# Optimization experiments

Hardware: AMD Instinct MI355X
Metric: run time of the kernel (lower is better)

## Reference

```python
import jax, jax.numpy as jnp
import numpy as np
import math

B, S, D, H, DFF, NB = 16, 512, 512, 8, 2048, 2
DK = D // H
L = 3 * NB  # NB blocks_1 layers + 2*NB blocks_2 layers
NEG = -1e32
LN_EPS = 1e-5


def _layernorm(x, g, b):
    mu = jnp.mean(x, -1, keepdims=True)
    var = jnp.mean((x - mu) ** 2, -1, keepdims=True)
    return (x - mu) * jax.lax.rsqrt(var + LN_EPS) * g + b


def _attention(q, k, v, mask, gamma, zero_pad):
    # q,k,v: [B,H,S,DK]; mask: [S,S] bool; gamma: [H]
    scores = jnp.einsum('bhid,bhjd->bhij', q, k) / math.sqrt(DK)
    maskf = mask.astype(scores.dtype)
    # no-grad distance-decay block (torch.no_grad + .detach())
    p = jax.nn.softmax(jnp.where(mask, scores, NEG), axis=-1) * maskf
    distcum = jnp.cumsum(p, axis=-1)
    disttot = jnp.sum(p, axis=-1, keepdims=True)
    idx = jnp.arange(S, dtype=scores.dtype)
    pos = jnp.abs(idx[None, :] - idx[:, None])  # |i-j|, [S,S]
    dist = jnp.sqrt(jnp.clip((disttot - distcum) * pos, 0.0, None))
    dist = jax.lax.stop_gradient(dist)
    g = -jax.nn.softplus(gamma)[None, :, None, None]  # [1,H,1,1]
    total_effect = jnp.clip(jnp.exp(dist * g), 1e-5, 1e5)
    scores = jnp.where(mask, scores * total_effect, NEG)
    attn = jax.nn.softmax(scores, axis=-1)
    if zero_pad:
        attn = attn.at[:, :, 0, :].set(0.0)
    return jnp.einsum('bhij,bhjd->bhid', attn, v)


def _mha(q, k, v, mask, zero_pad, Wk, bk, Wv, bv, Wo, bo, gam):
    # kq_same=True: queries also use the k projection
    def proj(x, W, b):
        return (x @ W + b).reshape(B, S, H, DK).transpose(0, 2, 1, 3)
    qh = proj(q, Wk, bk)
    kh = proj(k, Wk, bk)
    vh = proj(v, Wv, bv)
    out = _attention(qh, kh, vh, mask, gam, zero_pad)
    out = out.transpose(0, 2, 1, 3).reshape(B, S, D)
    return out @ Wo + bo


def _layer(mask_flag, query, key_, values, apply_pos, p):
    (Wk, bk, Wv, bv, Wo, bo, gam, g1, bn1, W1, bf1, W2, bf2, g2, bn2) = p
    idx = jnp.arange(S)
    if mask_flag == 1:
        mask = idx[None, :] <= idx[:, None]  # peek current + past
    else:
        mask = idx[None, :] < idx[:, None]   # strictly past
    zero_pad = (mask_flag == 0)
    q2 = _mha(query, key_, values, mask, zero_pad, Wk, bk, Wv, bv, Wo, bo, gam)
    query = _layernorm(query + q2, g1, bn1)
    if apply_pos:
        q2 = jax.nn.relu(query @ W1 + bf1) @ W2 + bf2
        query = _layernorm(query + q2, g2, bn2)
    return query


def _forward(q_embed_data, qa_embed_data, pid_embed_data, params):
    # emb_type='qid' (no 'pdiff') -> pid_embed_data unused inside attention
    def pslice(l):
        return tuple(a[l] for a in params)
    y = qa_embed_data
    x = q_embed_data
    for l in range(NB):  # blocks_1: self-attn on y, mask=1
        y = _layer(1, y, y, y, True, pslice(l))
    for i in range(NB):  # blocks_2: alternating (mask=1, no FFN) / (mask=0, values=y)
        x = _layer(1, x, x, x, False, pslice(NB + 2 * i))
        x = _layer(0, x, x, y, True, pslice(NB + 2 * i + 1))
    return x, y


def setup_inputs() -> dict:
    key = jax.random.key(0)
    ks = jax.random.split(key, 10)
    sD = 1.0 / math.sqrt(D)
    sF = 1.0 / math.sqrt(DFF)
    f32 = jnp.float32
    return {
        'q_embed_data': jax.random.normal(ks[0], (B, S, D), f32),
        'qa_embed_data': jax.random.normal(ks[1], (B, S, D), f32),
        'pid_embed_data': jax.random.normal(ks[2], (B, S, D), f32),
        'Wk': jax.random.normal(ks[3], (L, D, D), f32) * sD,
        'bk': jnp.zeros((L, D), f32),
        'Wv': jax.random.normal(ks[4], (L, D, D), f32) * sD,
        'bv': jnp.zeros((L, D), f32),
        'Wo': jax.random.normal(ks[5], (L, D, D), f32) * sD,
        'bo': jnp.zeros((L, D), f32),
        'gammas': jax.random.normal(ks[6], (L, H), f32) * 0.5,
        'ln1_g': jnp.ones((L, D), f32),
        'ln1_b': jnp.zeros((L, D), f32),
        'W1': jax.random.normal(ks[7], (L, D, DFF), f32) * sD,
        'b1': jnp.zeros((L, DFF), f32),
        'W2': jax.random.normal(ks[8], (L, DFF, D), f32) * sF,
        'b2': jnp.zeros((L, D), f32),
        'ln2_g': jnp.ones((L, D), f32),
        'ln2_b': jnp.zeros((L, D), f32),
    }


def reference(q_embed_data, qa_embed_data, pid_embed_data, Wk, bk, Wv, bv, Wo, bo,
              gammas, ln1_g, ln1_b, W1, b1, W2, b2, ln2_g, ln2_b):
    params = (Wk, bk, Wv, bv, Wo, bo, gammas, ln1_g, ln1_b, W1, b1, W2, b2, ln2_g, ln2_b)
    x, y = _forward(q_embed_data, qa_embed_data, pid_embed_data, params)
    return (x, y)
```

## Files before the change

### kernel.cpp

```cpp
#include <hip/hip_runtime.h>
#include <hip/hip_bf16.h>

#define Bsz  16
#define Sl   512
#define Dm   512
#define Hn   8
#define DKh  64
#define DFFn 2048
#define MROWS (Bsz * Sl)
#define NEGV (-1e32f)

typedef _Float16 f16;
typedef f16 f16x8 __attribute__((ext_vector_type(8)));
typedef f16 f16x4 __attribute__((ext_vector_type(4)));
typedef float f32x4 __attribute__((ext_vector_type(4)));

#define GLDS16(g, l) __builtin_amdgcn_global_load_lds( \
    (const __attribute__((address_space(1))) void*)(g), \
    (__attribute__((address_space(3))) void*)(l), 16, 0, 0)

__global__ void k_copy2(const float* __restrict__ in, float* __restrict__ out,
                        f16* __restrict__ outh, int n) {
    int i = blockIdx.x * 256 + threadIdx.x;
    if (i < n) { float v = in[i]; out[i] = v; outh[i] = (f16)v; }
}

__global__ void k_bcat(const float* __restrict__ bk, const float* __restrict__ bv,
                       float* __restrict__ bkv) {
    int i = blockIdx.x * 256 + threadIdx.x;
    int z = i >> 10, c = i & 1023;
    bkv[i] = (c < 512) ? bk[z * 512 + c] : bv[z * 512 + c - 512];
}

__global__ __launch_bounds__(256) void k_wconv(const float* __restrict__ src,
        f16* __restrict__ dst, int K, int N, int lmap, size_t zstride)
{
    __shared__ float T[32][36];
    int z = blockIdx.z;
    int ls = lmap ? (z < 2 ? z : 2 * z - 1) : z;
    const float* S = src + (size_t)ls * K * N;
    f16* Dt = dst + (size_t)z * zstride;
    int n0 = blockIdx.x * 32, k0 = blockIdx.y * 32;
    int t = threadIdx.x;
    int r = t >> 3, c = (t & 7) * 4;
    float4 v = *(const float4*)(S + (size_t)(k0 + r) * N + n0 + c);
    T[r][c] = v.x; T[r][c + 1] = v.y; T[r][c + 2] = v.z; T[r][c + 3] = v.w;
    __syncthreads();
    int n = t >> 3, kq = (t & 7) * 4;
    f16x4 o = { (f16)T[kq][n], (f16)T[kq + 1][n], (f16)T[kq + 2][n], (f16)T[kq + 3][n] };
    *(f16x4*)(Dt + (size_t)(n0 + n) * K + k0 + kq) = o;
}

template <int RELU, int OUT16, int VTOUT, int BK64>
__global__ __launch_bounds__(256) void k_gemm(
    const f16* __restrict__ A, const f16* __restrict__ Bt,
    const float* __restrict__ bias, float* __restrict__ C, f16* __restrict__ Ch,
    int M, int N, int K)
{
    constexpr int HL = BK64 ? 2 : 1;
    constexpr int BUF = HL * 4096;
    __shared__ f16 As[2 * BUF];
    __shared__ f16 Bs[2 * BUF];
    int tid = threadIdx.x;
    int w = tid >> 6, lane = tid & 63;
    int ln = lane & 15, rg = lane >> 4;
    int wr = w >> 1, wc = w & 1;
    int m0 = blockIdx.y * 128, n0 = blockIdx.x * 128;

    int s0 = tid, s1 = 256 + tid;
    int r0s = s0 >> 2, c0s = ((s0 & 3) ^ ((s0 >> 3) & 3));
    int r1s = s1 >> 2, c1s = ((s1 & 3) ^ ((s1 >> 3) & 3));

    const f16* a0 = A + (size_t)(m0 + r0s) * K + c0s * 8;
    const f16* a1 = A + (size_t)(m0 + r1s) * K + c1s * 8;
    const f16* b0 = Bt + (size_t)(n0 + r0s) * K + c0s * 8;
    const f16* b1 = Bt + (size_t)(n0 + r1s) * K + c1s * 8;

    int cc8 = (rg ^ ((ln >> 1) & 3)) * 8;

    f32x4 acc[4][4] = {};

    int nk = K >> (BK64 ? 6 : 5);

    auto STAGE = [&](int nb, int kt) {
        f16* lA = As + nb * BUF + w * 512;
        f16* lB = Bs + nb * BUF + w * 512;
        GLDS16(a0 + kt, lA);
        GLDS16(a1 + kt, lA + 2048);
        GLDS16(b0 + kt, lB);
        GLDS16(b1 + kt, lB + 2048);
        if (BK64) {
            GLDS16(a0 + kt + 32, lA + 4096);
            GLDS16(a1 + kt + 32, lA + 4096 + 2048);
            GLDS16(b0 + kt + 32, lB + 4096);
            GLDS16(b1 + kt + 32, lB + 4096 + 2048);
        }
    };

    STAGE(0, 0);
    __syncthreads();

    int cur = 0;
    for (int t = 0; t < nk; ++t) {
        if (t + 1 < nk) STAGE(cur ^ 1, (t + 1) << (BK64 ? 6 : 5));

#pragma unroll
        for (int hh = 0; hh < HL; ++hh) {
            const f16* Ab = As + cur * BUF + hh * 4096;
            const f16* Bb = Bs + cur * BUF + hh * 4096;
            f16x8 af[4], bf[4];
#pragma unroll
            for (int i = 0; i < 4; ++i) {
                int m = wr * 64 + i * 16 + ln;
                af[i] = *(const f16x8*)(Ab + m * 32 + cc8);
                int nn = wc * 64 + i * 16 + ln;
                bf[i] = *(const f16x8*)(Bb + nn * 32 + cc8);
            }
#pragma unroll
            for (int i = 0; i < 4; ++i)
#pragma unroll
                for (int j = 0; j < 4; ++j)
                    acc[i][j] = __builtin_amdgcn_mfma_f32_16x16x32_f16(af[i], bf[j], acc[i][j], 0, 0, 0);
        }

        __syncthreads();
        cur ^= 1;
    }

#pragma unroll
    for (int j = 0; j < 4; ++j) {
        int col = n0 + wc * 64 + j * 16 + ln;
        float bj = bias[col];
#pragma unroll
        for (int i = 0; i < 4; ++i) {
            int rb = m0 + wr * 64 + i * 16 + rg * 4;
            if (VTOUT == 1) {
                int bq = rb >> 9, s = rb & 511;
                int hh = col >> 6, dk = col & 63;
                f16x4 o;
#pragma unroll
                for (int r = 0; r < 4; ++r) o[r] = (f16)(acc[i][j][r] + bj);
                *(f16x4*)(Ch + (((size_t)(bq * 8 + hh) * 64 + dk) << 9) + s) = o;
            } else if (VTOUT == 2) {
                if (n0 < 512) {
#pragma unroll
                    for (int r = 0; r < 4; ++r)
                        Ch[(size_t)(rb + r) * 512 + col] = (f16)(acc[i][j][r] + bj);
                } else {
                    f16* Cv = (f16*)C;
                    int colv = col - 512;
                    int bq = rb >> 9, s = rb & 511;
                    int hh = colv >> 6, dk = colv & 63;
                    f16x4 o;
#pragma unroll
                    for (int r = 0; r < 4; ++r) o[r] = (f16)(acc[i][j][r] + bj);
                    *(f16x4*)(Cv + (((size_t)(bq * 8 + hh) * 64 + dk) << 9) + s) = o;
                }
            } else {
#pragma unroll
                for (int r = 0; r < 4; ++r) {
                    float v = acc[i][j][r] + bj;
                    if (RELU) v = fmaxf(v, 0.f);
                    if (OUT16) Ch[(size_t)(rb + r) * N + col] = (f16)v;
                    else       C [(size_t)(rb + r) * N + col] = v;
                }
            }
        }
    }
}

template <int JTC>
__device__ __forceinline__ void attn_body(
    float (*Sc)[516], f16* Ph, const f16* Qbase, const f16* vbase, f16* ob,
    f16x8 aq0, f16x8 aq1, float g,
    int w, int lane, int ln, int rg, int i0, int maskflag)
{
#pragma unroll
    for (int ui = 0; ui < JTC; ++ui) {
        int u = w + ui * 4;
        const f16* kb = Qbase + (size_t)(u * 16 + ln) * Dm + rg * 8;
        f16x8 b0 = *(const f16x8*)(kb);
        f16x8 b1 = *(const f16x8*)(kb + 32);
        f32x4 c = {};
        c = __builtin_amdgcn_mfma_f32_16x16x32_f16(aq0, b0, c, 0, 0, 0);
        c = __builtin_amdgcn_mfma_f32_16x16x32_f16(aq1, b1, c, 0, 0, 0);
#pragma unroll
        for (int r = 0; r < 4; ++r)
            Sc[rg * 4 + r][u * 16 + ln] = c[r];
    }
    __syncthreads();

    int jbase = lane * JTC;
    int im = i0 + w * 4;

    float run[4];
#pragma unroll
    for (int q = 0; q < 4; ++q) {
        int jmax = maskflag ? (im + q) : (im + q - 1);
        float acc = 0.f;
#pragma unroll
        for (int k = 0; k < JTC; ++k) {
            int j = jbase + k;
            float s = (j <= jmax) ? Sc[w * 4 + q][j] * 0.125f : NEGV;
            acc += __expf(s);
        }
        run[q] = acc;
    }
    float sl[4] = { run[0], run[1], run[2], run[3] };
#pragma unroll
    for (int off = 1; off < 64; off <<= 1) {
        float n0 = __shfl_up(sl[0], off);
        float n1 = __shfl_up(sl[1], off);
        float n2 = __shfl_up(sl[2], off);
        float n3 = __shfl_up(sl[3], off);
        if (lane >= off) { sl[0] += n0; sl[1] += n1; sl[2] += n2; sl[3] += n3; }
    }

    float pe2s[4][JTC];
    float Z2[4];
#pragma unroll
    for (int q = 0; q < 4; ++q) {
        float excl = sl[q] - run[q];
        float Z = __shfl(sl[q], 63);
        float inv = 1.f / Z;
        int i = im + q;
        int jmax = maskflag ? i : (i - 1);
        float csum = 0.f, z2 = 0.f;
#pragma unroll
        for (int k = 0; k < JTC; ++k) {
            int j = jbase + k;
            float s = (j <= jmax) ? Sc[w * 4 + q][j] * 0.125f : NEGV;
            float pe = __expf(s);
            csum += pe;
            float rem = (Z - excl - csum) * inv;
            float pos = fabsf((float)(i - j));
            float dd = fmaxf(rem * pos, 0.f);
            float te = __expf(sqrtf(dd) * g);
            te = fminf(fmaxf(te, 1e-5f), 1e5f);
            float sc = (j <= jmax) ? s * te : NEGV;
            float pe2 = __expf(sc);
            pe2s[q][k] = pe2;
            z2 += pe2;
        }
        Z2[q] = z2;
    }
#pragma unroll
    for (int off = 32; off >= 1; off >>= 1) {
        Z2[0] += __shfl_xor(Z2[0], off);
        Z2[1] += __shfl_xor(Z2[1], off);
        Z2[2] += __shfl_xor(Z2[2], off);
        Z2[3] += __shfl_xor(Z2[3], off);
    }
    __syncthreads();

#pragma unroll
    for (int q = 0; q < 4; ++q) {
        int r = w * 4 + q;
        float inv2 = 1.f / Z2[q];
        int zp = (maskflag == 0) && (im + q == 0);
        if constexpr (JTC == 8) {
            int slot = (lane & ~7) | ((lane & 7) ^ (r & 7));
            f16x8 o8;
#pragma unroll
            for (int k = 0; k < 8; ++k)
                o8[k] = (f16)(zp ? 0.f : pe2s[q][k] * inv2);
            *(f16x8*)(Ph + r * 512 + slot * 8) = o8;
        } else if constexpr (JTC == 4) {
            int cj = lane >> 1;
            int slot = (cj & ~7) | ((cj & 7) ^ (r & 7));
            f16x4 o4;
#pragma unroll
            for (int k = 0; k < 4; ++k)
                o4[k] = (f16)(zp ? 0.f : pe2s[q][k] * inv2);
            *(f16x4*)(Ph + r * 512 + slot * 8 + (lane & 1) * 4) = o4;
        } else {
#pragma unroll
            for (int k = 0; k < JTC; ++k) {
                int j = jbase + k;
                int cj = j >> 3;
                int slot = (cj & ~7) | ((cj & 7) ^ (r & 7));
                Ph[r * 512 + slot * 8 + (j & 7)] =
                    (f16)(zp ? 0.f : pe2s[q][k] * inv2);
            }
        }
    }
    __syncthreads();

    f32x4 oa0 = {}, oa1 = {};
#pragma unroll
    for (int f = 0; f < 2 * JTC; ++f) {
        f16x8 bv = *(const f16x8*)(vbase + (f >> 1) * 64 + (f & 1) * 32);
        int c = (f >> 1) * 8 + (f & 1) * 4 + rg;
        int slot = (c & ~7) | ((c & 7) ^ (ln & 7));
        f16x8 ap = *(const f16x8*)(Ph + ln * 512 + slot * 8);
        if (f & 1) oa1 = __builtin_amdgcn_mfma_f32_16x16x32_f16(ap, bv, oa1, 0, 0, 0);
        else       oa0 = __builtin_amdgcn_mfma_f32_16x16x32_f16(ap, bv, oa0, 0, 0, 0);
    }
    f32x4 oa = oa0 + oa1;
#pragma unroll
    for (int r = 0; r < 4; ++r)
        ob[(size_t)r * Dm] = (f16)oa[r];
}

__global__ __launch_bounds__(256, 4) void k_attn(
    const f16* __restrict__ Qh, const f16* __restrict__ VT,
    f16* __restrict__ O, const float* __restrict__ gam, int maskflag)
{
    __shared__ float Sc[16][516];
    f16* Ph = (f16*)Sc;

    int tid = threadIdx.x;
    int w = tid >> 6, lane = tid & 63;
    int ln = lane & 15, rg = lane >> 4;

    int bid = blockIdx.x;
    int lbid = (bid & 7) * 512 + (bid >> 3);
    int tile = 31 - (lbid & 31);
    int bh = lbid >> 5;
    int b = bh >> 3, h = bh & 7;
    int i0 = tile * 16;
    int jtc = (tile >> 2) + 1;

    const f16* Qbase = Qh + ((size_t)b * Sl) * Dm + h * DKh;
    const f16* vbase = VT + ((size_t)bh * 64 + w * 16 + ln) * 512 + rg * 8;
    f16* ob = O + ((size_t)b * Sl + i0 + rg * 4) * Dm + h * DKh + w * 16 + ln;

    float gm = gam[h];
    float g = -((gm > 20.f) ? gm : log1pf(__expf(gm)));

    f16x8 aq0 = *(const f16x8*)(Qbase + (size_t)(i0 + ln) * Dm + rg * 8);
    f16x8 aq1 = *(const f16x8*)(Qbase + (size_t)(i0 + ln) * Dm + 32 + rg * 8);

    switch (jtc) {
    case 1: attn_body<1>(Sc, Ph, Qbase, vbase, ob, aq0, aq1, g, w, lane, ln, rg, i0, maskflag); break;
    case 2: attn_body<2>(Sc, Ph, Qbase, vbase, ob, aq0, aq1, g, w, lane, ln, rg, i0, maskflag); break;
    case 3: attn_body<3>(Sc, Ph, Qbase, vbase, ob, aq0, aq1, g, w, lane, ln, rg, i0, maskflag); break;
    case 4: attn_body<4>(Sc, Ph, Qbase, vbase, ob, aq0, aq1, g, w, lane, ln, rg, i0, maskflag); break;
    case 5: attn_body<5>(Sc, Ph, Qbase, vbase, ob, aq0, aq1, g, w, lane, ln, rg, i0, maskflag); break;
    case 6: attn_body<6>(Sc, Ph, Qbase, vbase, ob, aq0, aq1, g, w, lane, ln, rg, i0, maskflag); break;
    case 7: attn_body<7>(Sc, Ph, Qbase, vbase, ob, aq0, aq1, g, w, lane, ln, rg, i0, maskflag); break;
    default: attn_body<8>(Sc, Ph, Qbase, vbase, ob, aq0, aq1, g, w, lane, ln, rg, i0, maskflag); break;
    }
}

__global__ __launch_bounds__(256) void k_ln(
    const float* __restrict__ Xn, const float* __restrict__ Rr,
    const float* __restrict__ gw, const float* __restrict__ bw,
    float* __restrict__ Out, f16* __restrict__ Outh)
{
    int tid = threadIdx.x;
    int w = tid >> 6, lane = tid & 63;
    int row = blockIdx.x * 4 + w;
    const float* xr = Xn + (size_t)row * Dm;
    const float* rr = Rr + (size_t)row * Dm;
    int c0 = lane * 4, c1 = 256 + lane * 4;
    float4 va = *(const float4*)(xr + c0);
    float4 vb = *(const float4*)(xr + c1);
    float4 ra = *(const float4*)(rr + c0);
    float4 rb = *(const float4*)(rr + c1);
    va.x += ra.x; va.y += ra.y; va.z += ra.z; va.w += ra.w;
    vb.x += rb.x; vb.y += rb.y; vb.z += rb.z; vb.w += rb.w;
    float sum = va.x + va.y + va.z + va.w + vb.x + vb.y + vb.z + vb.w;
#pragma unroll
    for (int off = 32; off >= 1; off >>= 1) sum += __shfl_xor(sum, off);
    float mu = sum * (1.f / 512.f);
    float var = 0.f;
    {
        float d;
        d = va.x - mu; var += d * d;  d = va.y - mu; var += d * d;
        d = va.z - mu; var += d * d;  d = va.w - mu; var += d * d;
        d = vb.x - mu; var += d * d;  d = vb.y - mu; var += d * d;
        d = vb.z - mu; var += d * d;  d = vb.w - mu; var += d * d;
    }
#pragma unroll
    for (int off = 32; off >= 1; off >>= 1) var += __shfl_xor(var, off);
    float rs = rsqrtf(var * (1.f / 512.f) + 1e-5f);
    float4 ga = *(const float4*)(gw + c0);
    float4 gb = *(const float4*)(gw + c1);
    float4 ba = *(const float4*)(bw + c0);
    float4 bb = *(const float4*)(bw + c1);
    float4 oa, ob;
    oa.x = (va.x - mu) * rs * ga.x + ba.x;  oa.y = (va.y - mu) * rs * ga.y + ba.y;
    oa.z = (va.z - mu) * rs * ga.z + ba.z;  oa.w = (va.w - mu) * rs * ga.w + ba.w;
    ob.x = (vb.x - mu) * rs * gb.x + bb.x;  ob.y = (vb.y - mu) * rs * gb.y + bb.y;
    ob.z = (vb.z - mu) * rs * gb.z + bb.z;  ob.w = (vb.w - mu) * rs * gb.w + bb.w;
    float* orow = Out + (size_t)row * Dm;
    f16* ohrow = Outh + (size_t)row * Dm;
    *(float4*)(orow + c0) = oa;
    *(float4*)(orow + c1) = ob;
    f16x4 ha = { (f16)oa.x, (f16)oa.y, (f16)oa.z, (f16)oa.w };
    f16x4 hb = { (f16)ob.x, (f16)ob.y, (f16)ob.z, (f16)ob.w };
    *(f16x4*)(ohrow + c0) = ha;
    *(f16x4*)(ohrow + c1) = hb;
}

extern "C" void kernel_launch(void* const* d_in, const int* in_sizes, int n_in,
                              void* d_out, int out_size, void* d_ws, size_t ws_size,
                              hipStream_t stream)
{
    const float* q_emb  = (const float*)d_in[0];
    const float* qa_emb = (const float*)d_in[1];
    const float* Wk  = (const float*)d_in[3];
    const float* bk  = (const float*)d_in[4];
    const float* Wv  = (const float*)d_in[5];
    const float* bv  = (const float*)d_in[6];
    const float* Wo  = (const float*)d_in[7];
    const float* bo  = (const float*)d_in[8];
    const float* gam = (const float*)d_in[9];
    const float* l1g = (const float*)d_in[10];
    const float* l1b = (const float*)d_in[11];
    const float* W1  = (const float*)d_in[12];
    const float* b1  = (const float*)d_in[13];
    const float* W2  = (const float*)d_in[14];
    const float* b2  = (const float*)d_in[15];
    const float* l2g = (const float*)d_in[16];
    const float* l2b = (const float*)d_in[17];
    float* outp = (float*)d_out;

    const size_t NE  = (size_t)MROWS * Dm;
    const size_t WDD = (size_t)Dm * Dm;
    const size_t WDF = (size_t)Dm * DFFn;
    const size_t WKV = 2 * WDD;

    float* xbuf = (float*)d_ws;
    float* ybuf = xbuf + NE;
    float* t2   = ybuf + NE;
    f16* xh  = (f16*)(t2 + NE);
    f16* yh  = xh + NE;
    f16* R   = yh + NE;
    f16* qh  = R;
    f16* vt  = R + 2 * NE;
    f16* t1h = R + 3 * NE;
    f16* fbh = R;
    f16* wkvh = R + 4 * NE;
    f16* woh = wkvh + 6 * WKV;
    f16* w1h = woh + 6 * WDD;
    f16* w2h = w1h + 4 * WDF;
    float* bkv = (float*)(w2h + 4 * WDF);

    k_wconv<<<dim3(Dm / 32, Dm / 32, 6), 256, 0, stream>>>(Wk, wkvh, Dm, Dm, 0, WKV);
    k_wconv<<<dim3(Dm / 32, Dm / 32, 6), 256, 0, stream>>>(Wv, wkvh + WDD, Dm, Dm, 0, WKV);
    k_wconv<<<dim3(Dm / 32, Dm / 32, 6), 256, 0, stream>>>(Wo, woh, Dm, Dm, 0, WDD);
    k_wconv<<<dim3(DFFn / 32, Dm / 32, 4), 256, 0, stream>>>(W1, w1h, Dm, DFFn, 1, WDF);
    k_wconv<<<dim3(Dm / 32, DFFn / 32, 4), 256, 0, stream>>>(W2, w2h, DFFn, Dm, 1, WDF);
    k_bcat<<<24, 256, 0, stream>>>(bk, bv, bkv);

    const int n = (int)NE;
    k_copy2<<<n / 256, 256, 0, stream>>>(q_emb,  xbuf, xh, n);
    k_copy2<<<n / 256, 256, 0, stream>>>(qa_emb, ybuf, yh, n);

    auto gemm32 = [&](const f16* A, const f16* Bt, const float* bias, float* C,
                      int M, int N, int K) {
        k_gemm<0, 0, 0, 1><<<dim3(N / 128, M / 128), 256, 0, stream>>>(A, Bt, bias, C, nullptr, M, N, K);
    };

    auto layer = [&](int l, int maskflag, float* Xq, f16* Xqh, f16* Xvh,
                     bool apply_pos, float* finalOut) {
        if (Xqh == Xvh) {
            k_gemm<0, 1, 2, 1><<<dim3(1024 / 128, MROWS / 128), 256, 0, stream>>>(
                Xqh, wkvh + (size_t)l * WKV, bkv + l * 1024, (float*)vt, qh, MROWS, 1024, Dm);
        } else {
            k_gemm<0, 1, 0, 1><<<dim3(Dm / 128, MROWS / 128), 256, 0, stream>>>(
                Xqh, wkvh + (size_t)l * WKV, bk + l * Dm, nullptr, qh, MROWS, Dm, Dm);
            k_gemm<0, 1, 1, 1><<<dim3(Dm / 128, MROWS / 128), 256, 0, stream>>>(
                Xvh, wkvh + (size_t)l * WKV + WDD, bv + l * Dm, nullptr, vt, MROWS, Dm, Dm);
        }
        k_attn<<<Bsz * Hn * 32, 256, 0, stream>>>(qh, vt, t1h, gam + l * Hn, maskflag);
        gemm32(t1h, woh + (size_t)l * WDD, bo + l * Dm, t2, MROWS, Dm, Dm);
        if (apply_pos) {
            k_ln<<<MROWS / 4, 256, 0, stream>>>(t2, Xq, l1g + l * Dm, l1b + l * Dm, Xq, Xqh);
            int sl = (l < 2) ? l : ((l + 1) >> 1);
            k_gemm<1, 1, 0, 0><<<dim3(DFFn / 128, MROWS / 128), 256, 0, stream>>>(
                Xqh, w1h + (size_t)sl * WDF, b1 + l * DFFn, nullptr, fbh, MROWS, DFFn, Dm);
            k_gemm<0, 0, 0, 1><<<dim3(Dm / 128, MROWS / 128), 256, 0, stream>>>(
                fbh, w2h + (size_t)sl * WDF, b2 + l * Dm, t2, nullptr, MROWS, Dm, DFFn);
            k_ln<<<MROWS / 4, 256, 0, stream>>>(t2, Xq, l2g + l * Dm, l2b + l * Dm,
                                                finalOut ? finalOut : Xq, Xqh);
        } else {
            k_ln<<<MROWS / 4, 256, 0, stream>>>(t2, Xq, l1g + l * Dm, l1b + l * Dm,
                                                finalOut ? finalOut : Xq, Xqh);
        }
    };

    const size_t NEo = NE;
    layer(0, 1, ybuf, yh, yh, true, nullptr);
    layer(1, 1, ybuf, yh, yh, true, outp + NEo);
    layer(2, 1, xbuf, xh, xh, false, nullptr);
    layer(3, 0, xbuf, xh, yh, true, nullptr);
    layer(4, 1, xbuf, xh, xh, false, nullptr);
    layer(5, 0, xbuf, xh, yh, true, outp);
}
```

Before: 1.136 ms.

## Merge prep kernels, fuse split Q/V projection GEMMs, cache attention scores in registers

Eight setup launches (weight transpose/convert, bias concat, embedding copies) are merged into one flat-indexed prep kernel. For layers whose query and value inputs differ, the two separate projection GEMMs become one launch that picks its A matrix, weight and bias by block index. In attention, each lane's score row is read once from shared memory into registers with vector loads, and the masked exponentials are reused in the second pass instead of being reloaded and recomputed. This cuts launch overhead, shared-memory reads and repeated math, at the cost of more registers per thread in the attention kernel.

```diff
diff --git a/kernel.cpp b/kernel.cpp
--- a/kernel.cpp
+++ b/kernel.cpp
@@ -19,29 +19,21 @@
     (const __attribute__((address_space(1))) void*)(g), \
     (__attribute__((address_space(3))) void*)(l), 16, 0, 0)
 
-__global__ void k_copy2(const float* __restrict__ in, float* __restrict__ out,
-                        f16* __restrict__ outh, int n) {
-    int i = blockIdx.x * 256 + threadIdx.x;
-    if (i < n) { float v = in[i]; out[i] = v; outh[i] = (f16)v; }
-}
-
-__global__ void k_bcat(const float* __restrict__ bk, const float* __restrict__ bv,
-                       float* __restrict__ bkv) {
-    int i = blockIdx.x * 256 + threadIdx.x;
-    int z = i >> 10, c = i & 1023;
-    bkv[i] = (c < 512) ? bk[z * 512 + c] : bv[z * 512 + c - 512];
-}
-
-__global__ __launch_bounds__(256) void k_wconv(const float* __restrict__ src,
-        f16* __restrict__ dst, int K, int N, int lmap, size_t zstride)
-{
-    __shared__ float T[32][36];
-    int z = blockIdx.z;
+struct PrepArgs {
+    const float *Wk, *Wv, *Wo, *W1, *W2, *bk, *bv, *q_emb, *qa_emb;
+    f16 *wkvh, *woh, *w1h, *w2h;
+    float *bkv, *xbuf, *ybuf;
+    f16 *xh, *yh;
+};
+
+__device__ __forceinline__ void wconv_body(const float* src, f16* dst,
+        int K, int N, int lmap, size_t zstride, int z, int nx, int ny,
+        int t, float (*T)[36])
+{
     int ls = lmap ? (z < 2 ? z : 2 * z - 1) : z;
     const float* S = src + (size_t)ls * K * N;
     f16* Dt = dst + (size_t)z * zstride;
-    int n0 = blockIdx.x * 32, k0 = blockIdx.y * 32;
-    int t = threadIdx.x;
+    int n0 = nx * 32, k0 = ny * 32;
     int r = t >> 3, c = (t & 7) * 4;
     float4 v = *(const float4*)(S + (size_t)(k0 + r) * N + n0 + c);
     T[r][c] = v.x; T[r][c + 1] = v.y; T[r][c + 2] = v.z; T[r][c + 3] = v.w;
@@ -51,11 +43,53 @@
     *(f16x4*)(Dt + (size_t)(n0 + n) * K + k0 + kq) = o;
 }
 
+__global__ __launch_bounds__(256) void k_prep(PrepArgs a)
+{
+    __shared__ float T[32][36];
+    int id = blockIdx.x;
+    int t = threadIdx.x;
+    const size_t WDD = (size_t)Dm * Dm;
+    const size_t WDF = (size_t)Dm * DFFn;
+    const size_t WKV = 2 * WDD;
+
+    if (id < 4608) {
+        int which = id / 1536, rest = id % 1536;
+        int z = rest >> 8, r2 = rest & 255;
+        int nx = r2 & 15, ny = r2 >> 4;
+        if (which == 0)      wconv_body(a.Wk, a.wkvh,       Dm, Dm, 0, WKV, z, nx, ny, t, T);
+        else if (which == 1) wconv_body(a.Wv, a.wkvh + WDD, Dm, Dm, 0, WKV, z, nx, ny, t, T);
+        else                 wconv_body(a.Wo, a.woh,        Dm, Dm, 0, WDD, z, nx, ny, t, T);
+    } else if (id < 8704) {
+        int id2 = id - 4608;
+        int z = id2 >> 10, r2 = id2 & 1023;
+        int nx = r2 & 63, ny = r2 >> 6;
+        wconv_body(a.W1, a.w1h, Dm, DFFn, 1, WDF, z, nx, ny, t, T);
+    } else if (id < 12800) {
+        int id3 = id - 8704;
+        int z = id3 >> 10, r2 = id3 & 1023;
+        int nx = r2 & 15, ny = r2 >> 4;
+        wconv_body(a.W2, a.w2h, DFFn, Dm, 1, WDF, z, nx, ny, t, T);
+    } else if (id < 12824) {
+        int i = (id - 12800) * 256 + t;
+        int z = i >> 10, c = i & 1023;
+        a.bkv[i] = (c < 512) ? a.bk[z * 512 + c] : a.bv[z * 512 + c - 512];
+    } else if (id < 29208) {
+        int i = (id - 12824) * 256 + t;
+        float v = a.q_emb[i];
+        a.xbuf[i] = v; a.xh[i] = (f16)v;
+    } else {
+        int i = (id - 29208) * 256 + t;
+        float v = a.qa_emb[i];
+        a.ybuf[i] = v; a.yh[i] = (f16)v;
+    }
+}
+
 template <int RELU, int OUT16, int VTOUT, int BK64>
 __global__ __launch_bounds__(256) void k_gemm(
     const f16* __restrict__ A, const f16* __restrict__ Bt,
     const float* __restrict__ bias, float* __restrict__ C, f16* __restrict__ Ch,
-    int M, int N, int K)
+    int M, int N, int K,
+    const f16* __restrict__ A2, f16* __restrict__ Ch2)
 {
     constexpr int HL = BK64 ? 2 : 1;
     constexpr int BUF = HL * 4096;
@@ -65,16 +99,22 @@
     int w = tid >> 6, lane = tid & 63;
     int ln = lane & 15, rg = lane >> 4;
     int wr = w >> 1, wc = w & 1;
-    int m0 = blockIdx.y * 128, n0 = blockIdx.x * 128;
+    int m0 = blockIdx.y * 128;
+    int half = (VTOUT == 3) ? (blockIdx.x >> 2) : 0;
+    int n0 = (VTOUT == 3) ? (blockIdx.x & 3) * 128 : blockIdx.x * 128;
+
+    const f16* Ause = (VTOUT == 3 && half) ? A2 : A;
+    const f16* Btuse = (VTOUT == 3) ? Bt + (size_t)half * 512 * 512 : Bt;
+    const float* biasuse = (VTOUT == 3) ? bias + half * 512 : bias;
 
     int s0 = tid, s1 = 256 + tid;
     int r0s = s0 >> 2, c0s = ((s0 & 3) ^ ((s0 >> 3) & 3));
     int r1s = s1 >> 2, c1s = ((s1 & 3) ^ ((s1 >> 3) & 3));
 
-    const f16* a0 = A + (size_t)(m0 + r0s) * K + c0s * 8;
-    const f16* a1 = A + (size_t)(m0 + r1s) * K + c1s * 8;
-    const f16* b0 = Bt + (size_t)(n0 + r0s) * K + c0s * 8;
-    const f16* b1 = Bt + (size_t)(n0 + r1s) * K + c1s * 8;
+    const f16* a0 = Ause + (size_t)(m0 + r0s) * K + c0s * 8;
+    const f16* a1 = Ause + (size_t)(m0 + r1s) * K + c1s * 8;
+    const f16* b0 = Btuse + (size_t)(n0 + r0s) * K + c0s * 8;
+    const f16* b1 = Btuse + (size_t)(n0 + r1s) * K + c1s * 8;
 
     int cc8 = (rg ^ ((ln >> 1) & 3)) * 8;
 
@@ -130,7 +170,7 @@
 #pragma unroll
     for (int j = 0; j < 4; ++j) {
         int col = n0 + wc * 64 + j * 16 + ln;
-        float bj = bias[col];
+        float bj = biasuse[col];
 #pragma unroll
         for (int i = 0; i < 4; ++i) {
             int rb = m0 + wr * 64 + i * 16 + rg * 4;
@@ -156,6 +196,19 @@
                     for (int r = 0; r < 4; ++r) o[r] = (f16)(acc[i][j][r] + bj);
                     *(f16x4*)(Cv + (((size_t)(bq * 8 + hh) * 64 + dk) << 9) + s) = o;
                 }
+            } else if (VTOUT == 3) {
+                if (half == 0) {
+#pragma unroll
+                    for (int r = 0; r < 4; ++r)
+                        Ch[(size_t)(rb + r) * 512 + col] = (f16)(acc[i][j][r] + bj);
+                } else {
+                    int bq = rb >> 9, s = rb & 511;
+                    int hh = col >> 6, dk = col & 63;
+                    f16x4 o;
+#pragma unroll
+                    for (int r = 0; r < 4; ++r) o[r] = (f16)(acc[i][j][r] + bj);
+                    *(f16x4*)(Ch2 + (((size_t)(bq * 8 + hh) * 64 + dk) << 9) + s) = o;
+                }
             } else {
 #pragma unroll
                 for (int r = 0; r < 4; ++r) {
@@ -193,15 +246,30 @@
     int jbase = lane * JTC;
     int im = i0 + w * 4;
 
+    float ss[4][JTC];
     float run[4];
 #pragma unroll
     for (int q = 0; q < 4; ++q) {
+        const float* Srow = &Sc[w * 4 + q][0];
+        if constexpr (JTC == 8) {
+            float4 t0 = *(const float4*)(Srow + jbase);
+            float4 t1 = *(const float4*)(Srow + jbase + 4);
+            ss[q][0] = t0.x; ss[q][1] = t0.y; ss[q][2] = t0.z; ss[q][3] = t0.w;
+            ss[q][4] = t1.x; ss[q][5] = t1.y; ss[q][6] = t1.z; ss[q][7] = t1.w;
+        } else if constexpr (JTC == 4) {
+            float4 t0 = *(const float4*)(Srow + jbase);
+            ss[q][0] = t0.x; ss[q][1] = t0.y; ss[q][2] = t0.z; ss[q][3] = t0.w;
+        } else {
+#pragma unroll
+            for (int k = 0; k < JTC; ++k) ss[q][k] = Srow[jbase + k];
+        }
         int jmax = maskflag ? (im + q) : (im + q - 1);
         float acc = 0.f;
 #pragma unroll
         for (int k = 0; k < JTC; ++k) {
             int j = jbase + k;
-            float s = (j <= jmax) ? Sc[w * 4 + q][j] * 0.125f : NEGV;
+            float s = (j <= jmax) ? ss[q][k] * 0.125f : NEGV;
+            ss[q][k] = s;
             acc += __expf(s);
         }
         run[q] = acc;
@@ -216,7 +284,6 @@
         if (lane >= off) { sl[0] += n0; sl[1] += n1; sl[2] += n2; sl[3] += n3; }
     }
 
-    float pe2s[4][JTC];
     float Z2[4];
 #pragma unroll
     for (int q = 0; q < 4; ++q) {
@@ -224,22 +291,19 @@
         float Z = __shfl(sl[q], 63);
         float inv = 1.f / Z;
         int i = im + q;
-        int jmax = maskflag ? i : (i - 1);
         float csum = 0.f, z2 = 0.f;
 #pragma unroll
         for (int k = 0; k < JTC; ++k) {
             int j = jbase + k;
-            float s = (j <= jmax) ? Sc[w * 4 + q][j] * 0.125f : NEGV;
-            float pe = __expf(s);
-            csum += pe;
+            float s = ss[q][k];
+            csum += __expf(s);
             float rem = (Z - excl - csum) * inv;
             float pos = fabsf((float)(i - j));
             float dd = fmaxf(rem * pos, 0.f);
             float te = __expf(sqrtf(dd) * g);
             te = fminf(fmaxf(te, 1e-5f), 1e5f);
-            float sc = (j <= jmax) ? s * te : NEGV;
-            float pe2 = __expf(sc);
-            pe2s[q][k] = pe2;
+            float pe2 = __expf(s * te);
+            ss[q][k] = pe2;
             z2 += pe2;
         }
         Z2[q] = z2;
@@ -263,7 +327,7 @@
             f16x8 o8;
 #pragma unroll
             for (int k = 0; k < 8; ++k)
-                o8[k] = (f16)(zp ? 0.f : pe2s[q][k] * inv2);
+                o8[k] = (f16)(zp ? 0.f : ss[q][k] * inv2);
             *(f16x8*)(Ph + r * 512 + slot * 8) = o8;
         } else if constexpr (JTC == 4) {
             int cj = lane >> 1;
@@ -271,7 +335,7 @@
             f16x4 o4;
 #pragma unroll
             for (int k = 0; k < 4; ++k)
-                o4[k] = (f16)(zp ? 0.f : pe2s[q][k] * inv2);
+                o4[k] = (f16)(zp ? 0.f : ss[q][k] * inv2);
             *(f16x4*)(Ph + r * 512 + slot * 8 + (lane & 1) * 4) = o4;
         } else {
 #pragma unroll
@@ -280,7 +344,7 @@
                 int cj = j >> 3;
                 int slot = (cj & ~7) | ((cj & 7) ^ (r & 7));
                 Ph[r * 512 + slot * 8 + (j & 7)] =
-                    (f16)(zp ? 0.f : pe2s[q][k] * inv2);
+                    (f16)(zp ? 0.f : ss[q][k] * inv2);
             }
         }
     }
@@ -438,42 +502,37 @@
     f16* w2h = w1h + 4 * WDF;
     float* bkv = (float*)(w2h + 4 * WDF);
 
-    k_wconv<<<dim3(Dm / 32, Dm / 32, 6), 256, 0, stream>>>(Wk, wkvh, Dm, Dm, 0, WKV);
-    k_wconv<<<dim3(Dm / 32, Dm / 32, 6), 256, 0, stream>>>(Wv, wkvh + WDD, Dm, Dm, 0, WKV);
-    k_wconv<<<dim3(Dm / 32, Dm / 32, 6), 256, 0, stream>>>(Wo, woh, Dm, Dm, 0, WDD);
-    k_wconv<<<dim3(DFFn / 32, Dm / 32, 4), 256, 0, stream>>>(W1, w1h, Dm, DFFn, 1, WDF);
-    k_wconv<<<dim3(Dm / 32, DFFn / 32, 4), 256, 0, stream>>>(W2, w2h, DFFn, Dm, 1, WDF);
-    k_bcat<<<24, 256, 0, stream>>>(bk, bv, bkv);
-
-    const int n = (int)NE;
-    k_copy2<<<n / 256, 256, 0, stream>>>(q_emb,  xbuf, xh, n);
-    k_copy2<<<n / 256, 256, 0, stream>>>(qa_emb, ybuf, yh, n);
-
-    auto gemm32 = [&](const f16* A, const f16* Bt, const float* bias, float* C,
-                      int M, int N, int K) {
-        k_gemm<0, 0, 0, 1><<<dim3(N / 128, M / 128), 256, 0, stream>>>(A, Bt, bias, C, nullptr, M, N, K);
-    };
+    PrepArgs pa;
+    pa.Wk = Wk; pa.Wv = Wv; pa.Wo = Wo; pa.W1 = W1; pa.W2 = W2;
+    pa.bk = bk; pa.bv = bv; pa.q_emb = q_emb; pa.qa_emb = qa_emb;
+    pa.wkvh = wkvh; pa.woh = woh; pa.w1h = w1h; pa.w2h = w2h;
+    pa.bkv = bkv; pa.xbuf = xbuf; pa.ybuf = ybuf; pa.xh = xh; pa.yh = yh;
+    k_prep<<<45592, 256, 0, stream>>>(pa);
 
     auto layer = [&](int l, int maskflag, float* Xq, f16* Xqh, f16* Xvh,
                      bool apply_pos, float* finalOut) {
         if (Xqh == Xvh) {
             k_gemm<0, 1, 2, 1><<<dim3(1024 / 128, MROWS / 128), 256, 0, stream>>>(
-                Xqh, wkvh + (size_t)l * WKV, bkv + l * 1024, (float*)vt, qh, MROWS, 1024, Dm);
+                Xqh, wkvh + (size_t)l * WKV, bkv + l * 1024, (float*)vt, qh,
+                MROWS, 1024, Dm, nullptr, nullptr);
         } else {
-            k_gemm<0, 1, 0, 1><<<dim3(Dm / 128, MROWS / 128), 256, 0, stream>>>(
-                Xqh, wkvh + (size_t)l * WKV, bk + l * Dm, nullptr, qh, MROWS, Dm, Dm);
-            k_gemm<0, 1, 1, 1><<<dim3(Dm / 128, MROWS / 128), 256, 0, stream>>>(
-                Xvh, wkvh + (size_t)l * WKV + WDD, bv + l * Dm, nullptr, vt, MROWS, Dm, Dm);
+            k_gemm<0, 1, 3, 1><<<dim3(8, MROWS / 128), 256, 0, stream>>>(
+                Xqh, wkvh + (size_t)l * WKV, bkv + l * 1024, nullptr, qh,
+                MROWS, 512, Dm, Xvh, vt);
         }
         k_attn<<<Bsz * Hn * 32, 256, 0, stream>>>(qh, vt, t1h, gam + l * Hn, maskflag);
-        gemm32(t1h, woh + (size_t)l * WDD, bo + l * Dm, t2, MROWS, Dm, Dm);
+        k_gemm<0, 0, 0, 1><<<dim3(Dm / 128, MROWS / 128), 256, 0, stream>>>(
+            t1h, woh + (size_t)l * WDD, bo + l * Dm, t2, nullptr,
+            MROWS, Dm, Dm, nullptr, nullptr);
         if (apply_pos) {
             k_ln<<<MROWS / 4, 256, 0, stream>>>(t2, Xq, l1g + l * Dm, l1b + l * Dm, Xq, Xqh);
             int sl = (l < 2) ? l : ((l + 1) >> 1);
             k_gemm<1, 1, 0, 0><<<dim3(DFFn / 128, MROWS / 128), 256, 0, stream>>>(
-                Xqh, w1h + (size_t)sl * WDF, b1 + l * DFFn, nullptr, fbh, MROWS, DFFn, Dm);
+                Xqh, w1h + (size_t)sl * WDF, b1 + l * DFFn, nullptr, fbh,
+                MROWS, DFFn, Dm, nullptr, nullptr);
             k_gemm<0, 0, 0, 1><<<dim3(Dm / 128, MROWS / 128), 256, 0, stream>>>(
-                fbh, w2h + (size_t)sl * WDF, b2 + l * Dm, t2, nullptr, MROWS, Dm, DFFn);
+                fbh, w2h + (size_t)sl * WDF, b2 + l * Dm, t2, nullptr,
+                MROWS, Dm, DFFn, nullptr, nullptr);
             k_ln<<<MROWS / 4, 256, 0, stream>>>(t2, Xq, l2g + l * Dm, l2b + l * Dm,
                                                 finalOut ? finalOut : Xq, Xqh);
         } else {
```

Result: faster. 1.106 ms (-2.6%).
